# Kernel tuning notes

Hardware: AMD Instinct MI355X
Metric: run time of the kernel (lower is better)

The kernel has to match this reference:

```python
import jax, jax.numpy as jnp
import numpy as np

H = 8          # multihead_num (also groups of the Conv1d)
LN_EPS = 1e-5  # torch.nn.LayerNorm default


def _gconv(x, w):
    """Grouped Conv1d, kernel=3, stride=1, 'same' reflect padding, no bias.
    x: [B, C_in, L], w: [C_out, C_in//H, K] (torch OIH layout)."""
    xp = jnp.pad(x, ((0, 0), (0, 0), (1, 1)), mode='reflect')
    return jax.lax.conv_general_dilated(
        xp, w, window_strides=(1,), padding='VALID',
        feature_group_count=H, dimension_numbers=('NCH', 'OIH', 'NCH'))


def setup_inputs() -> dict:
    key = jax.random.key(0)
    ks = jax.random.split(key, 5)
    B, C, L = 8, 512, 1024
    q = jax.random.normal(ks[0], (B, C, L), jnp.float32)
    k = jax.random.normal(ks[1], (B, C, L), jnp.float32)
    # causal mask: 1 above the diagonal -> -1e9 subtracted pre-softmax
    mask = jnp.triu(jnp.ones((L, L), jnp.float32), k=1)
    # init_params: std = sqrt(2 / (C_out + C_in/groups))
    std = float(np.sqrt(2.0 / (C + C // H)))
    wq = jax.random.normal(ks[2], (C, C // H, 3), jnp.float32) * std
    wk = jax.random.normal(ks[3], (C, C // H, 3), jnp.float32) * std
    wv = jax.random.normal(ks[4], (C, C // H, 3), jnp.float32) * std
    gamma = jnp.ones((C,), jnp.float32)
    beta = jnp.zeros((C,), jnp.float32)
    return {"q": q, "k": k, "mask": mask, "wq": wq, "wk": wk, "wv": wv,
            "gamma": gamma, "beta": beta}


def reference(q, k, mask, wq, wk, wv, gamma, beta):
    init = q                               # residual branch, [B, C, L]
    B, C, L = q.shape
    D = C // H                             # head dim
    v = k                                  # inputs list of length 2 -> v = k

    qh = _gconv(q, wq).reshape(B, H, D, L)  # split(dim=1)+cat(dim=0) == head axis
    kh = _gconv(k, wk).reshape(B, H, D, L)
    vh = _gconv(v, wv).reshape(B, H, D, L)

    # scores: q^T k per head; NOTE: scaled by sqrt(multihead_num), as in source
    scores = jnp.einsum('bhdl,bhdm->bhlm', qh, kh) / jnp.sqrt(
        jnp.asarray(H, qh.dtype))
    scores = scores - 1e9 * mask           # mask broadcast over [B, H]
    att = jax.nn.softmax(scores, axis=-1)  # dropout p=0.0 -> identity

    # o = att @ v^T, then concat heads along channel (head-major order)
    o = jnp.einsum('bhlm,bhdm->blhd', att, vh).reshape(B, L, C)

    # residual add + LayerNorm over channel dim
    x = o + jnp.swapaxes(init, 1, 2)       # [B, L, C]
    mu = jnp.mean(x, axis=-1, keepdims=True)
    var = jnp.mean(jnp.square(x - mu), axis=-1, keepdims=True)
    y = (x - mu) * jax.lax.rsqrt(var + LN_EPS) * gamma + beta
    return jnp.swapaxes(y, 1, 2)           # [B, C, L]
```

## Files before the change

### kernel.cpp

```cpp
#include <hip/hip_runtime.h>
#include <math.h>

#define H 8
#define B 8
#define C 512
#define L 1024
#define D 64
#define LDK 72

typedef __attribute__((ext_vector_type(4))) float f32x4;
typedef __attribute__((ext_vector_type(16))) float f32x16;
typedef __attribute__((ext_vector_type(8))) short bf16x8;

static __device__ __forceinline__ short f2bf(float x) {
    union { float f; unsigned u; } v; v.f = x;
    unsigned r = v.u + 0x7FFFu + ((v.u >> 16) & 1u);
    return (short)(r >> 16);
}
static __device__ __forceinline__ short f2bf_fast(float x) {
    union { float f; unsigned u; } v; v.f = x;
    return (short)((v.u + 0x8000u) >> 16);
}
static __device__ __forceinline__ int pack2(short a, short b) {
    return (int)((unsigned short)a | ((unsigned)(unsigned short)b << 16));
}
static __device__ __forceinline__ float bfs2f(short v) {
    union { unsigned u; float f; } w; w.u = ((unsigned)(unsigned short)v) << 16;
    return w.f;
}
static __device__ __forceinline__ void async16(const void* g, void* s) {
    __builtin_amdgcn_global_load_lds(
        (const __attribute__((address_space(1))) int*)g,
        (__attribute__((address_space(3))) int*)s, 16, 0, 0);
}

__global__ __launch_bounds__(256) void wprep_kernel(
    const float* __restrict__ wq, const float* __restrict__ wk,
    const float* __restrict__ wv, short* __restrict__ wtg)
{
    int idx = blockIdx.x * 256 + threadIdx.x;
    int jj    = idx & 7;
    int quad  = (idx >> 3) & 3;
    int d     = (idx >> 5) & 63;
    int r     = idx >> 11;
    int khalf = r & 1;  r >>= 1;
    int t     = r % 3;  r /= 3;
    int h     = r & 7;
    int conv  = r >> 3;
    const float* w = (conv == 0) ? wq : (conv == 1) ? wk : wv;
    int j_in = khalf * 32 + quad * 8 + jj;
    float v = w[(h * 64 + d) * 192 + j_in * 3 + t];
    if (conv == 0) v *= 0.51012254f;
    wtg[idx] = f2bf(v);
}

__global__ __launch_bounds__(256) void conv_kernel(
    const float* __restrict__ q, const float* __restrict__ k,
    const short* __restrict__ wtg,
    short* __restrict__ qh, short* __restrict__ kh, short* __restrict__ vh)
{
    int bx   = blockIdx.x;
    int tile = bx & 15;
    int h    = (bx >> 4) & 7;
    int b    = (bx >> 7) & 7;
    int src  = bx >> 10;

    __shared__ __align__(16) short xT[66 * LDK];

    int l0  = tile * 64;
    int tid = threadIdx.x;
    int wave = tid >> 6, lane = tid & 63;
    int n = lane & 15, quad = lane >> 4;

    const float* x  = src ? k : q;
    const float* xb = x + (size_t)(b * C + h * 64) * L + l0;

    int c0 = src ? 1 : 0;
    const short* wb0 = wtg + (size_t)((c0 * 8 + h) * 3 * 2) * 2048;
    bf16x8 wf[3][2], wf2[3][2];
    #pragma unroll
    for (int t = 0; t < 3; t++)
        #pragma unroll
        for (int kk = 0; kk < 2; kk++)
            wf[t][kk] = *(const bf16x8*)(wb0 + (t * 2 + kk) * 2048
                                         + (wave * 16 + n) * 32 + quad * 8);
    if (src) {
        const short* wb1 = wtg + (size_t)((2 * 8 + h) * 3 * 2) * 2048;
        #pragma unroll
        for (int t = 0; t < 3; t++)
            #pragma unroll
            for (int kk = 0; kk < 2; kk++)
                wf2[t][kk] = *(const bf16x8*)(wb1 + (t * 2 + kk) * 2048
                                              + (wave * 16 + n) * 32 + quad * 8);
    }

    {
        #pragma unroll
        for (int s = 0; s < 4; s++) {
            int idx = tid + s * 256;
            int j = idx >> 4, seg = idx & 15;
            float4 v = *(const float4*)(xb + j * L + seg * 4);
            int p = 1 + seg * 4;
            xT[(p + 0) * LDK + j] = f2bf(v.x);
            xT[(p + 1) * LDK + j] = f2bf(v.y);
            xT[(p + 2) * LDK + j] = f2bf(v.z);
            xT[(p + 3) * LDK + j] = f2bf(v.w);
        }
        if (tid < 64) {
            int gl = (l0 == 0) ? 1 : (l0 - 1);
            xT[0 * LDK + tid] = f2bf(x[(size_t)(b * C + h * 64 + tid) * L + gl]);
        } else if (tid < 128) {
            int j2 = tid - 64;
            int gl = (l0 + 64 >= L) ? (L - 2) : (l0 + 64);
            xT[65 * LDK + j2] = f2bf(x[(size_t)(b * C + h * 64 + j2) * L + gl]);
        }
    }
    __syncthreads();

    f32x4 acc[4], acc2[4];
    #pragma unroll
    for (int bl = 0; bl < 4; bl++) {
        acc[bl]  = (f32x4){0.f, 0.f, 0.f, 0.f};
        acc2[bl] = (f32x4){0.f, 0.f, 0.f, 0.f};
    }

    #pragma unroll
    for (int bl = 0; bl < 4; bl++) {
        #pragma unroll
        for (int t = 0; t < 3; t++) {
            #pragma unroll
            for (int kk = 0; kk < 2; kk++) {
                bf16x8 bf = *(const bf16x8*)&xT[(bl * 16 + n + t) * LDK
                                                + kk * 32 + quad * 8];
                acc[bl] = __builtin_amdgcn_mfma_f32_16x16x32_bf16(
                    wf[t][kk], bf, acc[bl], 0, 0, 0);
                if (src)
                    acc2[bl] = __builtin_amdgcn_mfma_f32_16x16x32_bf16(
                        wf2[t][kk], bf, acc2[bl], 0, 0, 0);
            }
        }
    }

    int bhh = b * H + h;
    short* o1 = src ? kh : qh;
    {
        short* ob = o1 + ((size_t)(bhh * 16 + tile)) * 4096;
        int ch = wave * 2 + (quad >> 1);
        #pragma unroll
        for (int bl = 0; bl < 4; bl++) {
            int l = bl * 16 + n;
            int phys = ch ^ (l & 7);
            int2 v;
            v.x = pack2(f2bf(acc[bl][0]), f2bf(acc[bl][1]));
            v.y = pack2(f2bf(acc[bl][2]), f2bf(acc[bl][3]));
            *(int2*)&ob[l * 64 + phys * 8 + (quad & 1) * 4] = v;
        }
    }
    if (src) {
        __syncthreads();
        #pragma unroll
        for (int bl = 0; bl < 4; bl++)
            #pragma unroll
            for (int r = 0; r < 4; r++) {
                int d = wave * 16 + quad * 4 + r;
                int l = bl * 16 + n;
                int phys = (bl * 2 + (n >> 3)) ^ (d & 7);
                xT[d * 64 + phys * 8 + (n & 7)] = f2bf(acc2[bl][r]);
            }
        __syncthreads();
        short* vb = vh + ((size_t)(bhh * 16 + tile)) * 4096;
        #pragma unroll
        for (int jj = 0; jj < 2; jj++) {
            int i = tid + jj * 256;
            *(int4*)(vb + i * 8) = *(const int4*)&xT[i * 8];
        }
    }
}

__global__ __launch_bounds__(128, 2) void flash_kernel(
    const short* __restrict__ qh, const short* __restrict__ kh,
    const short* __restrict__ vh, short* __restrict__ ot)
{
    __shared__ __align__(16) short lds[20480];

    int bx = blockIdx.x;
    int bh = bx & 63;
    int qt = 15 - (bx >> 6);
    int h  = bh & 7, b = bh >> 3;

    int tid  = threadIdx.x;
    int wave = tid >> 6;
    int lane = tid & 63;
    int m    = lane & 31;
    int half = lane >> 5;
    int sw   = m & 7;

    const short* Qg    = qh + ((size_t)(bh * 16 + qt)) * 4096;
    const short* Kbase = kh + (size_t)bh * 65536;
    const short* Vbase = vh + (size_t)bh * 65536;

    #pragma unroll
    for (int s = 0; s < 4; s++) {
        int ci = s * 128 + tid;
        int lo = (s * 128 + wave * 64) * 8;
        async16((const int4*)Qg + ci,    lds + lo);
        async16((const int4*)Kbase + ci, lds + 4096 + lo);
        async16((const int4*)Vbase + ci, lds + 8192 + lo);
    }
    __syncthreads();

    int row_q = wave * 32 + m;

    bf16x8 qb[4];
    #pragma unroll
    for (int st = 0; st < 4; st++)
        qb[st] = *(const bf16x8*)&lds[row_q * 64 + (((half + 2 * st) ^ sw) * 8)];

    const bf16x8 ones = {16256,16256,16256,16256,16256,16256,16256,16256};

    f32x16 O0, O1, Lacc;
    #pragma unroll
    for (int r = 0; r < 16; r++) { O0[r] = 0.f; O1[r] = 0.f; Lacc[r] = 0.f; }

    for (int kt = 0; kt <= qt; kt++) {
        if (kt > 0) __syncthreads();
        if (kt < qt) {
            const short* Kg = Kbase + (size_t)(kt + 1) * 4096;
            const short* Vg = Vbase + (size_t)(kt + 1) * 4096;
            int koff = 4096 + ((kt + 1) & 1) * 8192;
            #pragma unroll
            for (int s = 0; s < 4; s++) {
                int ci = s * 128 + tid;
                int lo = (s * 128 + wave * 64) * 8;
                async16((const int4*)Kg + ci, lds + koff + lo);
                async16((const int4*)Vg + ci, lds + koff + 4096 + lo);
            }
        }
        const short* Kb = lds + 4096 + (kt & 1) * 8192;
        const short* Vb = Kb + 4096;

        f32x16 s0, s1;
        #pragma unroll
        for (int r = 0; r < 16; r++) { s0[r] = 0.f; s1[r] = 0.f; }
        #pragma unroll
        for (int st = 0; st < 4; st++) {
            int co = ((half + 2 * st) ^ sw) * 8;
            bf16x8 ka0 = *(const bf16x8*)&Kb[m * 64 + co];
            bf16x8 ka1 = *(const bf16x8*)&Kb[(32 + m) * 64 + co];
            s0 = __builtin_amdgcn_mfma_f32_32x32x16_bf16(ka0, qb[st], s0, 0, 0, 0);
            s1 = __builtin_amdgcn_mfma_f32_32x32x16_bf16(ka1, qb[st], s1, 0, 0, 0);
        }

        if (kt == qt) {
            #pragma unroll
            for (int r = 0; r < 16; r++) {
                int ko = (r & 3) + 8 * (r >> 2) + 4 * half;
                if (ko > row_q)      s0[r] = -INFINITY;
                if (32 + ko > row_q) s1[r] = -INFINITY;
            }
        }

        #pragma unroll
        for (int t = 0; t < 4; t++) {
            int2 v0, v1;
            v0.x = pack2(f2bf_fast(__builtin_amdgcn_exp2f(s0[4*t+0] - 20.f)),
                         f2bf_fast(__builtin_amdgcn_exp2f(s0[4*t+1] - 20.f)));
            v0.y = pack2(f2bf_fast(__builtin_amdgcn_exp2f(s0[4*t+2] - 20.f)),
                         f2bf_fast(__builtin_amdgcn_exp2f(s0[4*t+3] - 20.f)));
            v1.x = pack2(f2bf_fast(__builtin_amdgcn_exp2f(s1[4*t+0] - 20.f)),
                         f2bf_fast(__builtin_amdgcn_exp2f(s1[4*t+1] - 20.f)));
            v1.y = pack2(f2bf_fast(__builtin_amdgcn_exp2f(s1[4*t+2] - 20.f)),
                         f2bf_fast(__builtin_amdgcn_exp2f(s1[4*t+3] - 20.f)));
            *(int2*)&lds[row_q * 64 + ((t       ^ sw) * 8) + 4 * half] = v0;
            *(int2*)&lds[row_q * 64 + (((4 + t) ^ sw) * 8) + 4 * half] = v1;
        }

        bf16x8 pa[4];
        #pragma unroll
        for (int st = 0; st < 4; st++)
            pa[st] = *(const bf16x8*)&lds[row_q * 64 + (((half + 2 * st) ^ sw) * 8)];

        #pragma unroll
        for (int st = 0; st < 4; st++) {
            int co = ((half + 2 * st) ^ sw) * 8;
            bf16x8 vb0 = *(const bf16x8*)&Vb[m * 64 + co];
            bf16x8 vb1 = *(const bf16x8*)&Vb[(32 + m) * 64 + co];
            Lacc = __builtin_amdgcn_mfma_f32_32x32x16_bf16(pa[st], ones, Lacc, 0, 0, 0);
            O0   = __builtin_amdgcn_mfma_f32_32x32x16_bf16(pa[st], vb0,  O0,  0, 0, 0);
            O1   = __builtin_amdgcn_mfma_f32_32x32x16_bf16(pa[st], vb1,  O1,  0, 0, 0);
        }
    }

    float inv[16];
    #pragma unroll
    for (int r = 0; r < 16; r++) inv[r] = 1.f / Lacc[r];

    __syncthreads();
    short* Eb = lds + 4096;
    #pragma unroll
    for (int t = 0; t < 4; t++) {
        int qoff = 8 * t + 4 * half;
        int2 v0, v1;
        v0.x = pack2(f2bf_fast(O0[4*t+0] * inv[4*t+0]), f2bf_fast(O0[4*t+1] * inv[4*t+1]));
        v0.y = pack2(f2bf_fast(O0[4*t+2] * inv[4*t+2]), f2bf_fast(O0[4*t+3] * inv[4*t+3]));
        v1.x = pack2(f2bf_fast(O1[4*t+0] * inv[4*t+0]), f2bf_fast(O1[4*t+1] * inv[4*t+1]));
        v1.y = pack2(f2bf_fast(O1[4*t+2] * inv[4*t+2]), f2bf_fast(O1[4*t+3] * inv[4*t+3]));
        *(int2*)&Eb[m * 72        + wave * 32 + qoff] = v0;
        *(int2*)&Eb[(32 + m) * 72 + wave * 32 + qoff] = v1;
    }
    __syncthreads();
    #pragma unroll
    for (int jj = 0; jj < 4; jj++) {
        int i = tid + jj * 128;
        int d = i >> 3, seg = i & 7;
        int4 v = *(const int4*)&Eb[d * 72 + seg * 8];
        *(int4*)(ot + ((size_t)(b * C) + h * 64 + d) * L + qt * 64 + seg * 8) = v;
    }
}

__global__ __launch_bounds__(512) void ln_kernel(
    const short* __restrict__ ot, const float* __restrict__ q,
    const float* __restrict__ gamma, const float* __restrict__ beta,
    float* __restrict__ y)
{
    int bx = blockIdx.x;
    int tile = bx & 31;
    int b = bx >> 5;
    int l0 = tile * 32;
    int tid = threadIdx.x;
    int li_ = tid & 31, cs = tid >> 5;

    __shared__ float sp[16][33], ssp[16][33];
    __shared__ float mu_s[32], rs_s[32];

    size_t base = ((size_t)b * C + cs * 32) * L + l0 + li_;
    const short* otp = ot + base;
    const float* qp  = q + base;

    float xr[32];
    float s = 0.f, ss = 0.f;
    #pragma unroll
    for (int cc = 0; cc < 32; cc++) {
        float x = bfs2f(otp[(size_t)cc * L]) + qp[(size_t)cc * L];
        xr[cc] = x;
        s += x; ss += x * x;
    }
    sp[cs][li_] = s; ssp[cs][li_] = ss;
    __syncthreads();
    if (tid < 32) {
        float t1 = 0.f, t2 = 0.f;
        #pragma unroll
        for (int j = 0; j < 16; j++) { t1 += sp[j][tid]; t2 += ssp[j][tid]; }
        float mean = t1 * (1.f / 512.f);
        float var  = t2 * (1.f / 512.f) - mean * mean;
        mu_s[tid] = mean;
        rs_s[tid] = rsqrtf(var + 1e-5f);
    }
    __syncthreads();
    float mu = mu_s[li_], rs = rs_s[li_];
    float* yp = y + base;
    #pragma unroll
    for (int cc = 0; cc < 32; cc++) {
        int c = cs * 32 + cc;
        yp[(size_t)cc * L] = (xr[cc] - mu) * rs * gamma[c] + beta[c];
    }
}

extern "C" void kernel_launch(void* const* d_in, const int* in_sizes, int n_in,
                              void* d_out, int out_size, void* d_ws, size_t ws_size,
                              hipStream_t stream)
{
    const float* q     = (const float*)d_in[0];
    const float* k     = (const float*)d_in[1];
    const float* wq    = (const float*)d_in[3];
    const float* wk    = (const float*)d_in[4];
    const float* wv    = (const float*)d_in[5];
    const float* gamma = (const float*)d_in[6];
    const float* beta  = (const float*)d_in[7];
    float* y = (float*)d_out;

    const size_t N = (size_t)B * H * L * D;
    short* qh  = (short*)d_ws;
    short* kh  = qh + N;
    short* vh  = kh + N;
    short* ot  = vh + N;
    short* wtg = ot + N;

    wprep_kernel<<<1152, 256, 0, stream>>>(wq, wk, wv, wtg);
    conv_kernel<<<2 * B * H * (L / 64), 256, 0, stream>>>(q, k, wtg, qh, kh, vh);
    flash_kernel<<<B * H * (L / 64), 128, 0, stream>>>(qh, kh, vh, ot);
    ln_kernel<<<B * (L / 32), 512, 0, stream>>>(ot, q, gamma, beta, y);
}
```

Before: 140.5 us.

## Pair complementary causal query tiles per flash block for balanced work

Each flash block now handles two query tiles, p and 15-p, so every block walks exactly 17 key tiles in one continuous double-buffered loop. This replaces the 1024-block grid with 512 uniformly loaded blocks, aiming to remove the causal load imbalance and tail effect of the old largest-first ordering. It doubles the accumulator registers (launch bounds drop to 1 block per SIMD pair) and grows LDS, which reduces occupancy. The epilogue writes both tiles in sequence.

```diff
diff --git a/kernel.cpp b/kernel.cpp
--- a/kernel.cpp
+++ b/kernel.cpp
@@ -177,16 +177,76 @@
     }
 }
 
-__global__ __launch_bounds__(128, 2) void flash_kernel(
+static __device__ __forceinline__ void flash_tile(
+    short* lds, int Poff, const short* Kb, const short* Vb,
+    const bf16x8* qb, bool diag, int row_q, int m, int half, int sw,
+    f32x16& O0, f32x16& O1, f32x16& La)
+{
+    const bf16x8 ones = {16256,16256,16256,16256,16256,16256,16256,16256};
+
+    f32x16 s0, s1;
+    #pragma unroll
+    for (int r = 0; r < 16; r++) { s0[r] = 0.f; s1[r] = 0.f; }
+    #pragma unroll
+    for (int st = 0; st < 4; st++) {
+        int co = ((half + 2 * st) ^ sw) * 8;
+        bf16x8 ka0 = *(const bf16x8*)&Kb[m * 64 + co];
+        bf16x8 ka1 = *(const bf16x8*)&Kb[(32 + m) * 64 + co];
+        s0 = __builtin_amdgcn_mfma_f32_32x32x16_bf16(ka0, qb[st], s0, 0, 0, 0);
+        s1 = __builtin_amdgcn_mfma_f32_32x32x16_bf16(ka1, qb[st], s1, 0, 0, 0);
+    }
+
+    if (diag) {
+        #pragma unroll
+        for (int r = 0; r < 16; r++) {
+            int ko = (r & 3) + 8 * (r >> 2) + 4 * half;
+            if (ko > row_q)      s0[r] = -INFINITY;
+            if (32 + ko > row_q) s1[r] = -INFINITY;
+        }
+    }
+
+    #pragma unroll
+    for (int t = 0; t < 4; t++) {
+        int2 v0, v1;
+        v0.x = pack2(f2bf_fast(__builtin_amdgcn_exp2f(s0[4*t+0] - 20.f)),
+                     f2bf_fast(__builtin_amdgcn_exp2f(s0[4*t+1] - 20.f)));
+        v0.y = pack2(f2bf_fast(__builtin_amdgcn_exp2f(s0[4*t+2] - 20.f)),
+                     f2bf_fast(__builtin_amdgcn_exp2f(s0[4*t+3] - 20.f)));
+        v1.x = pack2(f2bf_fast(__builtin_amdgcn_exp2f(s1[4*t+0] - 20.f)),
+                     f2bf_fast(__builtin_amdgcn_exp2f(s1[4*t+1] - 20.f)));
+        v1.y = pack2(f2bf_fast(__builtin_amdgcn_exp2f(s1[4*t+2] - 20.f)),
+                     f2bf_fast(__builtin_amdgcn_exp2f(s1[4*t+3] - 20.f)));
+        *(int2*)&lds[Poff + row_q * 64 + ((t       ^ sw) * 8) + 4 * half] = v0;
+        *(int2*)&lds[Poff + row_q * 64 + (((4 + t) ^ sw) * 8) + 4 * half] = v1;
+    }
+
+    bf16x8 pa[4];
+    #pragma unroll
+    for (int st = 0; st < 4; st++)
+        pa[st] = *(const bf16x8*)&lds[Poff + row_q * 64 + (((half + 2 * st) ^ sw) * 8)];
+
+    #pragma unroll
+    for (int st = 0; st < 4; st++) {
+        int co = ((half + 2 * st) ^ sw) * 8;
+        bf16x8 vb0 = *(const bf16x8*)&Vb[m * 64 + co];
+        bf16x8 vb1 = *(const bf16x8*)&Vb[(32 + m) * 64 + co];
+        La = __builtin_amdgcn_mfma_f32_32x32x16_bf16(pa[st], ones, La, 0, 0, 0);
+        O0 = __builtin_amdgcn_mfma_f32_32x32x16_bf16(pa[st], vb0,  O0, 0, 0, 0);
+        O1 = __builtin_amdgcn_mfma_f32_32x32x16_bf16(pa[st], vb1,  O1, 0, 0, 0);
+    }
+}
+
+__global__ __launch_bounds__(128, 1) void flash_kernel(
     const short* __restrict__ qh, const short* __restrict__ kh,
     const short* __restrict__ vh, short* __restrict__ ot)
 {
-    __shared__ __align__(16) short lds[20480];
+    __shared__ __align__(16) short lds[24576];
 
     int bx = blockIdx.x;
-    int bh = bx & 63;
-    int qt = 15 - (bx >> 6);
+    int p  = bx & 7;
+    int bh = bx >> 3;
     int h  = bh & 7, b = bh >> 3;
+    int qtB = p, qtA = 15 - p;
 
     int tid  = threadIdx.x;
     int wave = tid >> 6;
@@ -195,7 +255,8 @@
     int half = lane >> 5;
     int sw   = m & 7;
 
-    const short* Qg    = qh + ((size_t)(bh * 16 + qt)) * 4096;
+    const short* QgB   = qh + ((size_t)(bh * 16 + qtB)) * 4096;
+    const short* QgA   = qh + ((size_t)(bh * 16 + qtA)) * 4096;
     const short* Kbase = kh + (size_t)bh * 65536;
     const short* Vbase = vh + (size_t)bh * 65536;
 
@@ -203,31 +264,38 @@
     for (int s = 0; s < 4; s++) {
         int ci = s * 128 + tid;
         int lo = (s * 128 + wave * 64) * 8;
-        async16((const int4*)Qg + ci,    lds + lo);
-        async16((const int4*)Kbase + ci, lds + 4096 + lo);
-        async16((const int4*)Vbase + ci, lds + 8192 + lo);
+        async16((const int4*)QgB + ci,   lds + lo);
+        async16((const int4*)QgA + ci,   lds + 4096 + lo);
+        async16((const int4*)Kbase + ci, lds + 8192 + lo);
+        async16((const int4*)Vbase + ci, lds + 12288 + lo);
     }
     __syncthreads();
 
     int row_q = wave * 32 + m;
 
-    bf16x8 qb[4];
-    #pragma unroll
-    for (int st = 0; st < 4; st++)
-        qb[st] = *(const bf16x8*)&lds[row_q * 64 + (((half + 2 * st) ^ sw) * 8)];
-
-    const bf16x8 ones = {16256,16256,16256,16256,16256,16256,16256,16256};
-
-    f32x16 O0, O1, Lacc;
-    #pragma unroll
-    for (int r = 0; r < 16; r++) { O0[r] = 0.f; O1[r] = 0.f; Lacc[r] = 0.f; }
-
-    for (int kt = 0; kt <= qt; kt++) {
-        if (kt > 0) __syncthreads();
-        if (kt < qt) {
-            const short* Kg = Kbase + (size_t)(kt + 1) * 4096;
-            const short* Vg = Vbase + (size_t)(kt + 1) * 4096;
-            int koff = 4096 + ((kt + 1) & 1) * 8192;
+    bf16x8 qbB[4], qbA[4];
+    #pragma unroll
+    for (int st = 0; st < 4; st++) {
+        int co = ((half + 2 * st) ^ sw) * 8;
+        qbB[st] = *(const bf16x8*)&lds[row_q * 64 + co];
+        qbA[st] = *(const bf16x8*)&lds[4096 + row_q * 64 + co];
+    }
+
+    f32x16 OB0, OB1, LB, OA0, OA1, LA;
+    #pragma unroll
+    for (int r = 0; r < 16; r++) {
+        OB0[r] = 0.f; OB1[r] = 0.f; LB[r] = 0.f;
+        OA0[r] = 0.f; OA1[r] = 0.f; LA[r] = 0.f;
+    }
+
+    for (int it = 0; it < 17; it++) {
+        if (it > 0) __syncthreads();
+        if (it < 16) {
+            int nit = it + 1;
+            int nkt = (nit <= p) ? nit : nit - p - 1;
+            const short* Kg = Kbase + (size_t)nkt * 4096;
+            const short* Vg = Vbase + (size_t)nkt * 4096;
+            int koff = 8192 + (nit & 1) * 8192;
             #pragma unroll
             for (int s = 0; s < 4; s++) {
                 int ci = s * 128 + tid;
@@ -236,85 +304,50 @@
                 async16((const int4*)Vg + ci, lds + koff + 4096 + lo);
             }
         }
-        const short* Kb = lds + 4096 + (kt & 1) * 8192;
+        const short* Kb = lds + 8192 + (it & 1) * 8192;
         const short* Vb = Kb + 4096;
 
-        f32x16 s0, s1;
-        #pragma unroll
-        for (int r = 0; r < 16; r++) { s0[r] = 0.f; s1[r] = 0.f; }
-        #pragma unroll
-        for (int st = 0; st < 4; st++) {
-            int co = ((half + 2 * st) ^ sw) * 8;
-            bf16x8 ka0 = *(const bf16x8*)&Kb[m * 64 + co];
-            bf16x8 ka1 = *(const bf16x8*)&Kb[(32 + m) * 64 + co];
-            s0 = __builtin_amdgcn_mfma_f32_32x32x16_bf16(ka0, qb[st], s0, 0, 0, 0);
-            s1 = __builtin_amdgcn_mfma_f32_32x32x16_bf16(ka1, qb[st], s1, 0, 0, 0);
-        }
-
-        if (kt == qt) {
-            #pragma unroll
-            for (int r = 0; r < 16; r++) {
-                int ko = (r & 3) + 8 * (r >> 2) + 4 * half;
-                if (ko > row_q)      s0[r] = -INFINITY;
-                if (32 + ko > row_q) s1[r] = -INFINITY;
-            }
-        }
-
+        bool isB = (it <= p);
+        if (isB)
+            flash_tile(lds, 0, Kb, Vb, qbB, it == p, row_q, m, half, sw,
+                       OB0, OB1, LB);
+        else
+            flash_tile(lds, 4096, Kb, Vb, qbA, it == 16, row_q, m, half, sw,
+                       OA0, OA1, LA);
+    }
+
+    short* Eb = lds + 8192;
+    #pragma unroll
+    for (int tile2 = 0; tile2 < 2; tile2++) {
+        f32x16& O0 = tile2 ? OA0 : OB0;
+        f32x16& O1 = tile2 ? OA1 : OB1;
+        f32x16& La = tile2 ? LA  : LB;
+        int qt = tile2 ? qtA : qtB;
+
+        float inv[16];
+        #pragma unroll
+        for (int r = 0; r < 16; r++) inv[r] = 1.f / La[r];
+
+        __syncthreads();
         #pragma unroll
         for (int t = 0; t < 4; t++) {
+            int qoff = 8 * t + 4 * half;
             int2 v0, v1;
-            v0.x = pack2(f2bf_fast(__builtin_amdgcn_exp2f(s0[4*t+0] - 20.f)),
-                         f2bf_fast(__builtin_amdgcn_exp2f(s0[4*t+1] - 20.f)));
-            v0.y = pack2(f2bf_fast(__builtin_amdgcn_exp2f(s0[4*t+2] - 20.f)),
-                         f2bf_fast(__builtin_amdgcn_exp2f(s0[4*t+3] - 20.f)));
-            v1.x = pack2(f2bf_fast(__builtin_amdgcn_exp2f(s1[4*t+0] - 20.f)),
-                         f2bf_fast(__builtin_amdgcn_exp2f(s1[4*t+1] - 20.f)));
-            v1.y = pack2(f2bf_fast(__builtin_amdgcn_exp2f(s1[4*t+2] - 20.f)),
-                         f2bf_fast(__builtin_amdgcn_exp2f(s1[4*t+3] - 20.f)));
-            *(int2*)&lds[row_q * 64 + ((t       ^ sw) * 8) + 4 * half] = v0;
-            *(int2*)&lds[row_q * 64 + (((4 + t) ^ sw) * 8) + 4 * half] = v1;
-        }
-
-        bf16x8 pa[4];
-        #pragma unroll
-        for (int st = 0; st < 4; st++)
-            pa[st] = *(const bf16x8*)&lds[row_q * 64 + (((half + 2 * st) ^ sw) * 8)];
-
-        #pragma unroll
-        for (int st = 0; st < 4; st++) {
-            int co = ((half + 2 * st) ^ sw) * 8;
-            bf16x8 vb0 = *(const bf16x8*)&Vb[m * 64 + co];
-            bf16x8 vb1 = *(const bf16x8*)&Vb[(32 + m) * 64 + co];
-            Lacc = __builtin_amdgcn_mfma_f32_32x32x16_bf16(pa[st], ones, Lacc, 0, 0, 0);
-            O0   = __builtin_amdgcn_mfma_f32_32x32x16_bf16(pa[st], vb0,  O0,  0, 0, 0);
-            O1   = __builtin_amdgcn_mfma_f32_32x32x16_bf16(pa[st], vb1,  O1,  0, 0, 0);
-        }
-    }
-
-    float inv[16];
-    #pragma unroll
-    for (int r = 0; r < 16; r++) inv[r] = 1.f / Lacc[r];
-
-    __syncthreads();
-    short* Eb = lds + 4096;
-    #pragma unroll
-    for (int t = 0; t < 4; t++) {
-        int qoff = 8 * t + 4 * half;
-        int2 v0, v1;
-        v0.x = pack2(f2bf_fast(O0[4*t+0] * inv[4*t+0]), f2bf_fast(O0[4*t+1] * inv[4*t+1]));
-        v0.y = pack2(f2bf_fast(O0[4*t+2] * inv[4*t+2]), f2bf_fast(O0[4*t+3] * inv[4*t+3]));
-        v1.x = pack2(f2bf_fast(O1[4*t+0] * inv[4*t+0]), f2bf_fast(O1[4*t+1] * inv[4*t+1]));
-        v1.y = pack2(f2bf_fast(O1[4*t+2] * inv[4*t+2]), f2bf_fast(O1[4*t+3] * inv[4*t+3]));
-        *(int2*)&Eb[m * 72        + wave * 32 + qoff] = v0;
-        *(int2*)&Eb[(32 + m) * 72 + wave * 32 + qoff] = v1;
-    }
-    __syncthreads();
-    #pragma unroll
-    for (int jj = 0; jj < 4; jj++) {
-        int i = tid + jj * 128;
-        int d = i >> 3, seg = i & 7;
-        int4 v = *(const int4*)&Eb[d * 72 + seg * 8];
-        *(int4*)(ot + ((size_t)(b * C) + h * 64 + d) * L + qt * 64 + seg * 8) = v;
+            v0.x = pack2(f2bf_fast(O0[4*t+0] * inv[4*t+0]), f2bf_fast(O0[4*t+1] * inv[4*t+1]));
+            v0.y = pack2(f2bf_fast(O0[4*t+2] * inv[4*t+2]), f2bf_fast(O0[4*t+3] * inv[4*t+3]));
+            v1.x = pack2(f2bf_fast(O1[4*t+0] * inv[4*t+0]), f2bf_fast(O1[4*t+1] * inv[4*t+1]));
+            v1.y = pack2(f2bf_fast(O1[4*t+2] * inv[4*t+2]), f2bf_fast(O1[4*t+3] * inv[4*t+3]));
+            *(int2*)&Eb[m * 72        + wave * 32 + qoff] = v0;
+            *(int2*)&Eb[(32 + m) * 72 + wave * 32 + qoff] = v1;
+        }
+        __syncthreads();
+        #pragma unroll
+        for (int jj = 0; jj < 4; jj++) {
+            int i = tid + jj * 128;
+            int d = i >> 3, seg = i & 7;
+            int4 v = *(const int4*)&Eb[d * 72 + seg * 8];
+            *(int4*)(ot + ((size_t)(b * C) + h * 64 + d) * L + qt * 64 + seg * 8) = v;
+        }
     }
 }
 
@@ -388,6 +421,6 @@
 
     wprep_kernel<<<1152, 256, 0, stream>>>(wq, wk, wv, wtg);
     conv_kernel<<<2 * B * H * (L / 64), 256, 0, stream>>>(q, k, wtg, qh, kh, vh);
-    flash_kernel<<<B * H * (L / 64), 128, 0, stream>>>(qh, kh, vh, ot);
+    flash_kernel<<<B * H * 8, 128, 0, stream>>>(qh, kh, vh, ot);
     ln_kernel<<<B * (L / 32), 512, 0, stream>>>(ot, q, gamma, beta, y);
 }
```

Measured after the change: 146.3 us. +4.2%, slower.
